# Performance work log

Hardware: AMD Instinct MI355X
Metric: run time of the kernel (lower is better)

## Reference

```python
import jax, jax.numpy as jnp
import numpy as np

N = 32768       # flattened residues (batch*seq)
DIM = 1024      # dim == channel (required by residual add)
NRES = 21       # amino-acid types
RECYCLES = 2


def _quat_to_rot(q):
    w, x, y, z = q[..., 0], q[..., 1], q[..., 2], q[..., 3]
    return jnp.stack([
        jnp.stack([1 - 2 * (y * y + z * z), 2 * (x * y - w * z), 2 * (x * z + w * y)], -1),
        jnp.stack([2 * (x * y + w * z), 1 - 2 * (x * x + z * z), 2 * (y * z - w * x)], -1),
        jnp.stack([2 * (x * z - w * y), 2 * (y * z + w * x), 1 - 2 * (x * x + y * y)], -1),
    ], -2)


def _rand_rigid(key, shape, tscale=1.0):
    # random valid rigid transforms as 4x4 homogeneous matrices
    kq, kt = jax.random.split(key)
    q = jax.random.normal(kq, shape + (4,), jnp.float32)
    q = q / jnp.linalg.norm(q, axis=-1, keepdims=True)
    rot = _quat_to_rot(q)
    t = jax.random.normal(kt, shape + (3,), jnp.float32) * tscale
    m = jnp.zeros(shape + (4, 4), jnp.float32)
    m = m.at[..., :3, :3].set(rot).at[..., :3, 3].set(t).at[..., 3, 3].set(1.0)
    return m


def setup_inputs():
    key = jax.random.key(0)
    ks = jax.random.split(key, 12)
    s = 1.0 / np.sqrt(DIM)
    return {
        "rep0": jax.random.normal(ks[0], (N, DIM), jnp.float32),
        "rep1": jax.random.normal(ks[1], (N, DIM), jnp.float32),
        "w_in": jax.random.normal(ks[2], (DIM, DIM), jnp.float32) * s,
        "b_in": jnp.zeros((DIM,), jnp.float32),
        "w1": jax.random.normal(ks[3], (DIM, DIM), jnp.float32) * s,
        "b1": jnp.zeros((DIM,), jnp.float32),
        "w2": jax.random.normal(ks[4], (DIM, DIM), jnp.float32) * s,
        "b2": jnp.zeros((DIM,), jnp.float32),
        "w_ang": jax.random.normal(ks[5], (DIM, 14), jnp.float32) * s,
        "b_ang": jnp.zeros((14,), jnp.float32),
        "rigids": _rand_rigid(ks[6], (N,), tscale=10.0),              # backbone frames
        "default_frames": _rand_rigid(ks[7], (NRES, 8), tscale=1.5), # restype_rigid_group_default_frame
        "lit_positions": jax.random.normal(ks[8], (NRES, 14, 3), jnp.float32),
        "atom_mask": (jax.random.uniform(ks[9], (NRES, 14)) > 0.2).astype(jnp.float32),
        "aatype": jax.random.randint(ks[10], (N,), 0, NRES),
        "group_idx": jax.random.randint(ks[11], (NRES, 14), 0, 8),   # restype_atom14_to_rigid_group
    }


def reference(rep0, rep1, w_in, b_in, w1, b1, w2, b2, w_ang, b_ang,
              rigids, default_frames, lit_positions, atom_mask, aatype, group_idx):
    # InputProjection: shared ReLU+Linear applied to each representation, summed
    act = (jax.nn.relu(rep0) @ w_in + b_in) + (jax.nn.relu(rep1) @ w_in + b_in)
    # ResidueBlock with residual recycles: act += Linear(ReLU(Linear(ReLU(act))))
    for _ in range(RECYCLES):
        h = jax.nn.relu(act) @ w1 + b1
        h = jax.nn.relu(h) @ w2 + b2
        act = act + h
    # TorisonAngles: Linear(dim,14) -> (N,7,2) -> l2_normalize
    ang = (jax.nn.relu(act) @ w_ang + b_ang).reshape(N, 7, 2)
    angles = ang / jnp.sqrt(jnp.maximum(jnp.sum(ang * ang, -1, keepdims=True), 1e-12))
    # torsion_angles_to_frames: prepend identity backbone angle (sin=0, cos=1)
    sin = jnp.concatenate([jnp.zeros((N, 1), angles.dtype), angles[..., 0]], 1)  # [N,8]
    cos = jnp.concatenate([jnp.ones((N, 1), angles.dtype), angles[..., 1]], 1)
    z = jnp.zeros_like(sin); one = jnp.ones_like(sin)
    rotx = jnp.stack([
        jnp.stack([one, z, z, z], -1),
        jnp.stack([z, cos, -sin, z], -1),
        jnp.stack([z, sin, cos, z], -1),
        jnp.stack([z, z, z, one], -1),
    ], -2)                                            # [N,8,4,4] rotation about x by torsion
    frames = default_frames[aatype] @ rotx            # [N,8,4,4]
    # chi2/chi3/chi4 frames are defined relative to the previous chi frame
    f5 = frames[:, 4] @ frames[:, 5]
    f6 = f5 @ frames[:, 6]
    f7 = f6 @ frames[:, 7]
    frames_to_bb = jnp.concatenate([frames[:, :5], jnp.stack([f5, f6, f7], 1)], 1)
    frames_global = rigids[:, None] @ frames_to_bb    # [N,8,4,4]
    # frames_and_literature_positions_to_atom14_pos
    gidx = group_idx[aatype]                          # [N,14] rigid-group id per atom
    f14 = jnp.take_along_axis(frames_global,
                              jnp.broadcast_to(gidx[:, :, None, None], (N, 14, 4, 4)),
                              axis=1)                 # [N,14,4,4]
    pos = lit_positions[aatype]                       # [N,14,3]
    pred = jnp.einsum('naij,naj->nai', f14[..., :3, :3], pos) + f14[..., :3, 3]
    pred = pred * atom_mask[aatype][..., None]        # [N,14,3]
    return angles, pred, frames_global
```

## Files before the change

kernel.cpp:

```cpp
#include <hip/hip_runtime.h>
#include <stdint.h>

typedef uint16_t u16;
typedef uint32_t u32;
typedef __bf16 bf16;
typedef bf16 bf16x8 __attribute__((ext_vector_type(8)));
typedef float f32x4 __attribute__((ext_vector_type(4)));

#define N_RES 32768
#define DIM 1024

__device__ __forceinline__ float b2f(u16 u) {
  u32 v = ((u32)u) << 16;
  float f;
  __builtin_memcpy(&f, &v, 4);
  return f;
}
__device__ __forceinline__ u16 f2b(float f) {
  u32 u;
  __builtin_memcpy(&u, &f, 4);
  u += 0x7fffu + ((u >> 16) & 1u);
  return (u16)(u >> 16);
}
__device__ __forceinline__ void split2(float v, u16& h, u16& l) {
  h = f2b(v);
  l = f2b(v - b2f(h));
}
__device__ __forceinline__ void relu_mask4(uint4& h, uint4& l) {
  u32 s, m;
  s = h.x & 0x80008000u; m = ((s >> 15) & 0x00010001u) * 0xFFFFu; h.x &= ~m; l.x &= ~m;
  s = h.y & 0x80008000u; m = ((s >> 15) & 0x00010001u) * 0xFFFFu; h.y &= ~m; l.y &= ~m;
  s = h.z & 0x80008000u; m = ((s >> 15) & 0x00010001u) * 0xFFFFu; h.z &= ~m; l.z &= ~m;
  s = h.w & 0x80008000u; m = ((s >> 15) & 0x00010001u) * 0xFFFFu; h.w &= ~m; l.w &= ~m;
}
__device__ __forceinline__ void relu_split8(bf16x8& h, bf16x8& l) {
  uint4 uh, ul;
  __builtin_memcpy(&uh, &h, 16);
  __builtin_memcpy(&ul, &l, 16);
  relu_mask4(uh, ul);
  __builtin_memcpy(&h, &uh, 16);
  __builtin_memcpy(&l, &ul, 16);
}
__device__ __forceinline__ void split8(const float* v, uint4& H, uint4& L) {
  u16 h[8], l[8];
#pragma unroll
  for (int i = 0; i < 8; ++i) split2(v[i], h[i], l[i]);
  H.x = (u32)h[0] | ((u32)h[1] << 16);
  H.y = (u32)h[2] | ((u32)h[3] << 16);
  H.z = (u32)h[4] | ((u32)h[5] << 16);
  H.w = (u32)h[6] | ((u32)h[7] << 16);
  L.x = (u32)l[0] | ((u32)l[1] << 16);
  L.y = (u32)l[2] | ((u32)l[3] << 16);
  L.z = (u32)l[4] | ((u32)l[5] << 16);
  L.w = (u32)l[6] | ((u32)l[7] << 16);
}

__device__ __forceinline__ void g2l16(const void* g, void* lds) {
  __builtin_amdgcn_global_load_lds(
      (__attribute__((address_space(1))) void*)(g),
      (__attribute__((address_space(3))) void*)(lds), 16, 0, 0);
}

__global__ __launch_bounds__(256) void transpose_split(const float* __restrict__ in,
                                                       u16* __restrict__ outh,
                                                       u16* __restrict__ outl) {
  __shared__ float t[32][33];
  const int bx = blockIdx.x * 32, by = blockIdx.y * 32;
  const int tx = threadIdx.x, ty = threadIdx.y;
  for (int i = ty; i < 32; i += 8) t[i][tx] = in[(size_t)(by + i) * DIM + bx + tx];
  __syncthreads();
  for (int i = ty; i < 32; i += 8) {
    u16 h, l;
    split2(t[tx][i], h, l);
    const size_t o = (size_t)(bx + i) * DIM + by + tx;
    outh[o] = h;
    outl[o] = l;
  }
}

__global__ __launch_bounds__(256) void prep_input(const float* __restrict__ rep0,
                                                  const float* __restrict__ rep1,
                                                  u16* __restrict__ oh,
                                                  u16* __restrict__ ol) {
  const size_t base = ((size_t)blockIdx.x * 256 + threadIdx.x) * 8;
  float4 x0 = *(const float4*)(rep0 + base);
  float4 x1 = *(const float4*)(rep0 + base + 4);
  float4 y0 = *(const float4*)(rep1 + base);
  float4 y1 = *(const float4*)(rep1 + base + 4);
  float v[8];
  v[0] = fmaxf(x0.x, 0.f) + fmaxf(y0.x, 0.f);
  v[1] = fmaxf(x0.y, 0.f) + fmaxf(y0.y, 0.f);
  v[2] = fmaxf(x0.z, 0.f) + fmaxf(y0.z, 0.f);
  v[3] = fmaxf(x0.w, 0.f) + fmaxf(y0.w, 0.f);
  v[4] = fmaxf(x1.x, 0.f) + fmaxf(y1.x, 0.f);
  v[5] = fmaxf(x1.y, 0.f) + fmaxf(y1.y, 0.f);
  v[6] = fmaxf(x1.z, 0.f) + fmaxf(y1.z, 0.f);
  v[7] = fmaxf(x1.w, 0.f) + fmaxf(y1.w, 0.f);
  uint4 H, L;
  split8(v, H, L);
  *(uint4*)(oh + base) = H;
  *(uint4*)(ol + base) = L;
}

__global__ __launch_bounds__(256, 2) void gemm_split(
    const u16* __restrict__ Ah, const u16* __restrict__ Al, int reluA,
    const u16* __restrict__ Bh, const u16* __restrict__ Bl,
    const float* __restrict__ bias, float bscale,
    const u16* __restrict__ Rh, const u16* __restrict__ Rl,
    u16* __restrict__ Oh, u16* __restrict__ Ol) {
  __shared__ __align__(16) u16 Ash[128 * 32];
  __shared__ __align__(16) u16 Asl[128 * 32];
  __shared__ __align__(16) u16 Bsh[128 * 32];
  __shared__ __align__(16) u16 Bsl[128 * 32];
  const int tid = threadIdx.x;
  const int wave = tid >> 6;
  const int lane = tid & 63;
  const int lrow = lane & 15;
  const int lquad = lane >> 4;

  const int g = blockIdx.x + (blockIdx.y << 3);
  const int xcd = g & 7;
  const int j = g >> 3;
  const int bm = (xcd * 32 + (j >> 3)) * 128;
  const int bn = (j & 7) * 128;

  const int wm = (wave & 1) * 64;
  const int wn = (wave >> 1) * 64;

  f32x4 acc[4][4];
#pragma unroll
  for (int i = 0; i < 4; ++i)
#pragma unroll
    for (int jj = 0; jj < 4; ++jj) acc[i][jj] = (f32x4){0.f, 0.f, 0.f, 0.f};

  const int r0 = tid >> 2;
  const int c0 = tid & 3;
  const u16* pAh0 = Ah + (size_t)(bm + r0) * DIM + c0 * 8;
  const u16* pAh1 = Ah + (size_t)(bm + 64 + r0) * DIM + c0 * 8;
  const u16* pAl0 = Al + (size_t)(bm + r0) * DIM + c0 * 8;
  const u16* pAl1 = Al + (size_t)(bm + 64 + r0) * DIM + c0 * 8;
  const u16* pBh0 = Bh + (size_t)(bn + r0) * DIM + c0 * 8;
  const u16* pBh1 = Bh + (size_t)(bn + 64 + r0) * DIM + c0 * 8;
  const u16* pBl0 = Bl + (size_t)(bn + r0) * DIM + c0 * 8;
  const u16* pBl1 = Bl + (size_t)(bn + 64 + r0) * DIM + c0 * 8;
  u16* dA0 = Ash + (size_t)tid * 8;
  u16* dA1 = Ash + (size_t)(tid + 256) * 8;
  u16* dAl0 = Asl + (size_t)tid * 8;
  u16* dAl1 = Asl + (size_t)(tid + 256) * 8;
  u16* dB0 = Bsh + (size_t)tid * 8;
  u16* dB1 = Bsh + (size_t)(tid + 256) * 8;
  u16* dBl0 = Bsl + (size_t)tid * 8;
  u16* dBl1 = Bsl + (size_t)(tid + 256) * 8;

  for (int kb = 0; kb < DIM; kb += 32) {
    g2l16(pAh0 + kb, dA0);
    g2l16(pAh1 + kb, dA1);
    g2l16(pAl0 + kb, dAl0);
    g2l16(pAl1 + kb, dAl1);
    g2l16(pBh0 + kb, dB0);
    g2l16(pBh1 + kb, dB1);
    g2l16(pBl0 + kb, dBl0);
    g2l16(pBl1 + kb, dBl1);
    __syncthreads();

    bf16x8 a_h[4], a_l[4], b_h[4], b_l[4];
#pragma unroll
    for (int i = 0; i < 4; ++i) {
      a_h[i] = *(const bf16x8*)(Ash + (wm + i * 16 + lrow) * 32 + lquad * 8);
      a_l[i] = *(const bf16x8*)(Asl + (wm + i * 16 + lrow) * 32 + lquad * 8);
      if (reluA) relu_split8(a_h[i], a_l[i]);
    }
#pragma unroll
    for (int jj = 0; jj < 4; ++jj) {
      b_h[jj] = *(const bf16x8*)(Bsh + (wn + jj * 16 + lrow) * 32 + lquad * 8);
      b_l[jj] = *(const bf16x8*)(Bsl + (wn + jj * 16 + lrow) * 32 + lquad * 8);
    }
#pragma unroll
    for (int i = 0; i < 4; ++i)
#pragma unroll
      for (int jj = 0; jj < 4; ++jj) {
        acc[i][jj] = __builtin_amdgcn_mfma_f32_16x16x32_bf16(a_h[i], b_h[jj], acc[i][jj], 0, 0, 0);
        acc[i][jj] = __builtin_amdgcn_mfma_f32_16x16x32_bf16(a_h[i], b_l[jj], acc[i][jj], 0, 0, 0);
        acc[i][jj] = __builtin_amdgcn_mfma_f32_16x16x32_bf16(a_l[i], b_h[jj], acc[i][jj], 0, 0, 0);
      }
    __syncthreads();
  }

#pragma unroll
  for (int jj = 0; jj < 4; ++jj) {
    const int col = bn + wn + jj * 16 + lrow;
    const float bj = bias[col] * bscale;
#pragma unroll
    for (int i = 0; i < 4; ++i) {
      const int row0 = bm + wm + i * 16 + lquad * 4;
#pragma unroll
      for (int r = 0; r < 4; ++r) {
        const size_t idx = (size_t)(row0 + r) * DIM + col;
        float v = acc[i][jj][r] + bj;
        if (Rh) v += b2f(Rh[idx]) + b2f(Rl[idx]);
        u16 h, l;
        split2(v, h, l);
        Oh[idx] = h;
        Ol[idx] = l;
      }
    }
  }
}

__global__ __launch_bounds__(256) void angles_split(
    const u16* __restrict__ ACTh, const u16* __restrict__ ACTl,
    const u16* __restrict__ WAh, const u16* __restrict__ WAl,
    const float* __restrict__ b_ang, float* __restrict__ out_angles) {
  const int tid = threadIdx.x;
  const int wave = tid >> 6, lane = tid & 63;
  const int lrow = lane & 15, lquad = lane >> 4;
  const int rowA = blockIdx.x * 64 + wave * 16 + lrow;
  f32x4 acc = (f32x4){0.f, 0.f, 0.f, 0.f};
  const u16* gah = ACTh + (size_t)rowA * DIM + lquad * 8;
  const u16* gal = ACTl + (size_t)rowA * DIM + lquad * 8;
  const u16* gbh = WAh + (size_t)lrow * DIM + lquad * 8;
  const u16* gbl = WAl + (size_t)lrow * DIM + lquad * 8;
#pragma unroll 4
  for (int kb = 0; kb < DIM; kb += 32) {
    bf16x8 ah = *(const bf16x8*)(gah + kb);
    bf16x8 al = *(const bf16x8*)(gal + kb);
    relu_split8(ah, al);
    bf16x8 bh = *(const bf16x8*)(gbh + kb);
    bf16x8 bl = *(const bf16x8*)(gbl + kb);
    acc = __builtin_amdgcn_mfma_f32_16x16x32_bf16(ah, bh, acc, 0, 0, 0);
    acc = __builtin_amdgcn_mfma_f32_16x16x32_bf16(ah, bl, acc, 0, 0, 0);
    acc = __builtin_amdgcn_mfma_f32_16x16x32_bf16(al, bh, acc, 0, 0, 0);
  }
  const int col = lrow;
  const float bj = (col < 14) ? b_ang[col] : 0.f;
#pragma unroll
  for (int r = 0; r < 4; ++r) {
    float v = acc[r] + bj;
    float p = __shfl_xor(v, 1, 64);
    float s2 = fmaxf(v * v + p * p, 1e-12f);
    float o = v * rsqrtf(s2);
    const int orow = blockIdx.x * 64 + wave * 16 + lquad * 4 + r;
    if (col < 14) out_angles[(size_t)orow * 14 + col] = o;
  }
}

__global__ __launch_bounds__(256) void prep_wang(const float* __restrict__ w,
                                                 u16* __restrict__ outh,
                                                 u16* __restrict__ outl) {
  for (int idx = threadIdx.x; idx < 16 * 1024; idx += 256) {
    const int n = idx & 15;
    const int k = idx >> 4;
    const float v = (n < 14) ? w[(size_t)k * 14 + n] : 0.f;
    u16 h, l;
    split2(v, h, l);
    outh[(size_t)n * DIM + k] = h;
    outl[(size_t)n * DIM + k] = l;
  }
}

__device__ __forceinline__ void mm34(const float* A, const float* B, float* O) {
#pragma unroll
  for (int r = 0; r < 3; ++r) {
#pragma unroll
    for (int c = 0; c < 4; ++c) {
      float v = A[r * 4 + 0] * B[0 * 4 + c] + A[r * 4 + 1] * B[1 * 4 + c] +
                A[r * 4 + 2] * B[2 * 4 + c];
      if (c == 3) v += A[r * 4 + 3];
      O[r * 4 + c] = v;
    }
  }
}

__global__ __launch_bounds__(256) void frames_kernel(
    const float* __restrict__ angles, const float* __restrict__ rigids,
    const float* __restrict__ dframes, const float* __restrict__ litpos,
    const float* __restrict__ amask, const int* __restrict__ aatype,
    const int* __restrict__ gidx, float* __restrict__ out_pred,
    float* __restrict__ out_frames) {
  const int n = blockIdx.x * 256 + threadIdx.x;
  const int aa = aatype[n];

  float fr[8][12];
  const float* angp = angles + (size_t)n * 14;
#pragma unroll
  for (int g = 0; g < 8; ++g) {
    float s, c;
    if (g == 0) { s = 0.f; c = 1.f; }
    else { s = angp[(g - 1) * 2]; c = angp[(g - 1) * 2 + 1]; }
    const float* D = dframes + ((size_t)aa * 8 + g) * 16;
#pragma unroll
    for (int r = 0; r < 3; ++r) {
      float d0 = D[r * 4 + 0], d1 = D[r * 4 + 1], d2 = D[r * 4 + 2], d3 = D[r * 4 + 3];
      fr[g][r * 4 + 0] = d0;
      fr[g][r * 4 + 1] = d1 * c + d2 * s;
      fr[g][r * 4 + 2] = d2 * c - d1 * s;
      fr[g][r * 4 + 3] = d3;
    }
  }
  float tmp[12];
  mm34(fr[4], fr[5], tmp);
#pragma unroll
  for (int e = 0; e < 12; ++e) fr[5][e] = tmp[e];
  mm34(fr[5], fr[6], tmp);
#pragma unroll
  for (int e = 0; e < 12; ++e) fr[6][e] = tmp[e];
  mm34(fr[6], fr[7], tmp);
#pragma unroll
  for (int e = 0; e < 12; ++e) fr[7][e] = tmp[e];

  float R[12];
  const float* rp = rigids + (size_t)n * 16;
#pragma unroll
  for (int e = 0; e < 12; ++e) R[e] = rp[e];
#pragma unroll
  for (int g = 0; g < 8; ++g) {
    mm34(R, fr[g], tmp);
#pragma unroll
    for (int e = 0; e < 12; ++e) fr[g][e] = tmp[e];
  }

  float4* of = (float4*)(out_frames + (size_t)n * 128);
#pragma unroll
  for (int g = 0; g < 8; ++g) {
    of[g * 4 + 0] = (float4){fr[g][0], fr[g][1], fr[g][2], fr[g][3]};
    of[g * 4 + 1] = (float4){fr[g][4], fr[g][5], fr[g][6], fr[g][7]};
    of[g * 4 + 2] = (float4){fr[g][8], fr[g][9], fr[g][10], fr[g][11]};
    of[g * 4 + 3] = (float4){0.f, 0.f, 0.f, 1.f};
  }

  float P[42];
#pragma unroll
  for (int a = 0; a < 14; ++a) {
    const int g = gidx[aa * 14 + a];
    float f[12];
#pragma unroll
    for (int q = 0; q < 8; ++q) {
      if (q == 0) {
#pragma unroll
        for (int e = 0; e < 12; ++e) f[e] = fr[0][e];
      } else {
        const bool sel = (g == q);
#pragma unroll
        for (int e = 0; e < 12; ++e) f[e] = sel ? fr[q][e] : f[e];
      }
    }
    const float px = litpos[((size_t)aa * 14 + a) * 3 + 0];
    const float py = litpos[((size_t)aa * 14 + a) * 3 + 1];
    const float pz = litpos[((size_t)aa * 14 + a) * 3 + 2];
    const float mk = amask[aa * 14 + a];
    P[a * 3 + 0] = (f[0] * px + f[1] * py + f[2] * pz + f[3]) * mk;
    P[a * 3 + 1] = (f[4] * px + f[5] * py + f[6] * pz + f[7]) * mk;
    P[a * 3 + 2] = (f[8] * px + f[9] * py + f[10] * pz + f[11]) * mk;
  }
  float2* op = (float2*)(out_pred + (size_t)n * 42);
#pragma unroll
  for (int i = 0; i < 21; ++i) op[i] = (float2){P[2 * i], P[2 * i + 1]};
}

__global__ __launch_bounds__(256) void ws_diag(float* __restrict__ out, float mb) {
  const int i = blockIdx.x * 256 + threadIdx.x;
  if (i < N_RES * 14) out[i] = mb;
}

extern "C" void kernel_launch(void* const* d_in, const int* in_sizes, int n_in,
                              void* d_out, int out_size, void* d_ws, size_t ws_size,
                              hipStream_t stream) {
  const float* rep0 = (const float*)d_in[0];
  const float* rep1 = (const float*)d_in[1];
  const float* w_in = (const float*)d_in[2];
  const float* b_in = (const float*)d_in[3];
  const float* w1 = (const float*)d_in[4];
  const float* b1 = (const float*)d_in[5];
  const float* w2 = (const float*)d_in[6];
  const float* b2 = (const float*)d_in[7];
  const float* w_ang = (const float*)d_in[8];
  const float* b_ang = (const float*)d_in[9];
  const float* rigids = (const float*)d_in[10];
  const float* dframes = (const float*)d_in[11];
  const float* litpos = (const float*)d_in[12];
  const float* amask = (const float*)d_in[13];
  const int* aatype = (const int*)d_in[14];
  const int* gidx = (const int*)d_in[15];

  const size_t SLOT = (size_t)N_RES * DIM;
  const size_t NEED_U16 = 4 * SLOT + 6 * (size_t)DIM * DIM + 2 * 16 * DIM;

  float* out_ang = (float*)d_out;
  float* out_pred = out_ang + (size_t)N_RES * 14;
  float* out_frames = out_pred + (size_t)N_RES * 42;

  if (ws_size < NEED_U16 * 2) {
    ws_diag<<<(N_RES * 14 + 255) / 256, 256, 0, stream>>>(
        out_ang, (float)(ws_size >> 20));
    return;
  }

  u16* ACTh = (u16*)d_ws;
  u16* ACTl = ACTh + SLOT;
  u16* Hh = ACTl + SLOT;
  u16* Hl = Hh + SLOT;
  u16* W0h = Hl + SLOT;
  u16* W0l = W0h + (size_t)DIM * DIM;
  u16* W1h = W0l + (size_t)DIM * DIM;
  u16* W1l = W1h + (size_t)DIM * DIM;
  u16* W2h = W1l + (size_t)DIM * DIM;
  u16* W2l = W2h + (size_t)DIM * DIM;
  u16* WAh = W2l + (size_t)DIM * DIM;
  u16* WAl = WAh + (size_t)16 * DIM;

  transpose_split<<<dim3(32, 32), dim3(32, 8), 0, stream>>>(w_in, W0h, W0l);
  transpose_split<<<dim3(32, 32), dim3(32, 8), 0, stream>>>(w1, W1h, W1l);
  transpose_split<<<dim3(32, 32), dim3(32, 8), 0, stream>>>(w2, W2h, W2l);
  prep_wang<<<1, 256, 0, stream>>>(w_ang, WAh, WAl);

  prep_input<<<(N_RES * DIM / 8) / 256, 256, 0, stream>>>(rep0, rep1, Hh, Hl);

  dim3 gg(DIM / 128, N_RES / 128);
  gemm_split<<<gg, 256, 0, stream>>>(Hh, Hl, 0, W0h, W0l, b_in, 2.f,
                                     nullptr, nullptr, ACTh, ACTl);
  gemm_split<<<gg, 256, 0, stream>>>(ACTh, ACTl, 1, W1h, W1l, b1, 1.f,
                                     nullptr, nullptr, Hh, Hl);
  gemm_split<<<gg, 256, 0, stream>>>(Hh, Hl, 1, W2h, W2l, b2, 1.f,
                                     ACTh, ACTl, ACTh, ACTl);
  gemm_split<<<gg, 256, 0, stream>>>(ACTh, ACTl, 1, W1h, W1l, b1, 1.f,
                                     nullptr, nullptr, Hh, Hl);
  gemm_split<<<gg, 256, 0, stream>>>(Hh, Hl, 1, W2h, W2l, b2, 1.f,
                                     ACTh, ACTl, ACTh, ACTl);

  angles_split<<<N_RES / 64, 256, 0, stream>>>(ACTh, ACTl, WAh, WAl, b_ang,
                                               out_ang);
  frames_kernel<<<N_RES / 256, 256, 0, stream>>>(out_ang, rigids, dframes, litpos,
                                                 amask, aatype, gidx, out_pred,
                                                 out_frames);
}
```

Baseline: 1.753 ms.

## Double-buffer split-bf16 GEMM LDS tiles with XOR-swizzled interleaved hi/lo layout

The GEMM main loop now uses two LDS buffers and issues the global-to-LDS copies for the next K tile before computing on the current one. This lets load latency overlap the MFMA work and drops one barrier per iteration. The hi and lo halves are interleaved into 64-wide rows with an XOR swizzle to reduce LDS bank conflicts on the fragment reads. LDS use doubles, which may limit occupancy with two blocks per CU, and the swizzle addressing has to match exactly on both the write and read sides.

```diff
diff --git a/kernel.cpp b/kernel.cpp
--- a/kernel.cpp
+++ b/kernel.cpp
@@ -108,10 +108,8 @@
     const float* __restrict__ bias, float bscale,
     const u16* __restrict__ Rh, const u16* __restrict__ Rl,
     u16* __restrict__ Oh, u16* __restrict__ Ol) {
-  __shared__ __align__(16) u16 Ash[128 * 32];
-  __shared__ __align__(16) u16 Asl[128 * 32];
-  __shared__ __align__(16) u16 Bsh[128 * 32];
-  __shared__ __align__(16) u16 Bsl[128 * 32];
+  __shared__ __align__(16) u16 AS[2][128 * 64];
+  __shared__ __align__(16) u16 BS[2][128 * 64];
   const int tid = threadIdx.x;
   const int wave = tid >> 6;
   const int lane = tid & 63;
@@ -133,47 +131,56 @@
 #pragma unroll
     for (int jj = 0; jj < 4; ++jj) acc[i][jj] = (f32x4){0.f, 0.f, 0.f, 0.f};
 
-  const int r0 = tid >> 2;
-  const int c0 = tid & 3;
-  const u16* pAh0 = Ah + (size_t)(bm + r0) * DIM + c0 * 8;
-  const u16* pAh1 = Ah + (size_t)(bm + 64 + r0) * DIM + c0 * 8;
-  const u16* pAl0 = Al + (size_t)(bm + r0) * DIM + c0 * 8;
-  const u16* pAl1 = Al + (size_t)(bm + 64 + r0) * DIM + c0 * 8;
-  const u16* pBh0 = Bh + (size_t)(bn + r0) * DIM + c0 * 8;
-  const u16* pBh1 = Bh + (size_t)(bn + 64 + r0) * DIM + c0 * 8;
-  const u16* pBl0 = Bl + (size_t)(bn + r0) * DIM + c0 * 8;
-  const u16* pBl1 = Bl + (size_t)(bn + 64 + r0) * DIM + c0 * 8;
-  u16* dA0 = Ash + (size_t)tid * 8;
-  u16* dA1 = Ash + (size_t)(tid + 256) * 8;
-  u16* dAl0 = Asl + (size_t)tid * 8;
-  u16* dAl1 = Asl + (size_t)(tid + 256) * 8;
-  u16* dB0 = Bsh + (size_t)tid * 8;
-  u16* dB1 = Bsh + (size_t)(tid + 256) * 8;
-  u16* dBl0 = Bsl + (size_t)tid * 8;
-  u16* dBl1 = Bsl + (size_t)(tid + 256) * 8;
-
-  for (int kb = 0; kb < DIM; kb += 32) {
-    g2l16(pAh0 + kb, dA0);
-    g2l16(pAh1 + kb, dA1);
-    g2l16(pAl0 + kb, dAl0);
-    g2l16(pAl1 + kb, dAl1);
-    g2l16(pBh0 + kb, dB0);
-    g2l16(pBh1 + kb, dB1);
-    g2l16(pBl0 + kb, dBl0);
-    g2l16(pBl1 + kb, dBl1);
-    __syncthreads();
-
+  const int srow = tid >> 3;
+  const int dc = (tid & 7) ^ (srow & 7);
+  const size_t scol = (size_t)(dc & 3) * 8;
+  const u16* srcA = ((dc < 4) ? Ah : Al) + (size_t)(bm + srow) * DIM + scol;
+  const u16* srcB = ((dc < 4) ? Bh : Bl) + (size_t)(bn + srow) * DIM + scol;
+  u16* dA0 = &AS[0][0] + tid * 8;
+  u16* dA1 = &AS[1][0] + tid * 8;
+  u16* dB0 = &BS[0][0] + tid * 8;
+  u16* dB1 = &BS[1][0] + tid * 8;
+
+  const int swzH = ((lquad ^ (lrow & 7)) * 8);
+  const int swzL = swzH ^ 32;
+
+#define STAGE(BUFA, BUFB, KT)                                        \
+  {                                                                  \
+    const size_t ko = (size_t)(KT) * 32;                             \
+    _Pragma("unroll") for (int is = 0; is < 4; ++is) {               \
+      g2l16(srcA + ko + (size_t)is * 32 * DIM, (BUFA) + is * 2048);  \
+      g2l16(srcB + ko + (size_t)is * 32 * DIM, (BUFB) + is * 2048);  \
+    }                                                                \
+  }
+
+  STAGE(dA0, dB0, 0);
+  __syncthreads();
+
+  int cur = 0;
+  for (int kt = 0; kt < 32; ++kt) {
+    if (kt + 1 < 32) {
+      if (cur == 0) {
+        STAGE(dA1, dB1, kt + 1);
+      } else {
+        STAGE(dA0, dB0, kt + 1);
+      }
+    }
+
+    const u16* As = &AS[cur][0];
+    const u16* Bs = &BS[cur][0];
     bf16x8 a_h[4], a_l[4], b_h[4], b_l[4];
 #pragma unroll
     for (int i = 0; i < 4; ++i) {
-      a_h[i] = *(const bf16x8*)(Ash + (wm + i * 16 + lrow) * 32 + lquad * 8);
-      a_l[i] = *(const bf16x8*)(Asl + (wm + i * 16 + lrow) * 32 + lquad * 8);
+      const u16* arow = As + (wm + i * 16 + lrow) * 64;
+      a_h[i] = *(const bf16x8*)(arow + swzH);
+      a_l[i] = *(const bf16x8*)(arow + swzL);
       if (reluA) relu_split8(a_h[i], a_l[i]);
     }
 #pragma unroll
     for (int jj = 0; jj < 4; ++jj) {
-      b_h[jj] = *(const bf16x8*)(Bsh + (wn + jj * 16 + lrow) * 32 + lquad * 8);
-      b_l[jj] = *(const bf16x8*)(Bsl + (wn + jj * 16 + lrow) * 32 + lquad * 8);
+      const u16* brow = Bs + (wn + jj * 16 + lrow) * 64;
+      b_h[jj] = *(const bf16x8*)(brow + swzH);
+      b_l[jj] = *(const bf16x8*)(brow + swzL);
     }
 #pragma unroll
     for (int i = 0; i < 4; ++i)
@@ -184,7 +191,9 @@
         acc[i][jj] = __builtin_amdgcn_mfma_f32_16x16x32_bf16(a_l[i], b_h[jj], acc[i][jj], 0, 0, 0);
       }
     __syncthreads();
-  }
+    cur ^= 1;
+  }
+#undef STAGE
 
 #pragma unroll
   for (int jj = 0; jj < 4; ++jj) {
```

New measurement: 1.783 ms. About the same (+1.7%).
